# Optimization experiments

Hardware: AMD Instinct MI355X
Metric: run time of the kernel (lower is better)

## Reference

```python
import jax, jax.numpy as jnp
import numpy as np

G, K, H = 4, 8, 512  # gate_dim, k blocks, block size

def setup_inputs() -> dict:
    key = jax.random.key(0)
    kx, kA, kB = jax.random.split(key, 3)
    x = jax.random.normal(kx, (4096, K * H), dtype=jnp.float32)
    # xavier_normal for (h,h) matrices: std = sqrt(2/(h+h)) = 1/sqrt(h)
    std = 1.0 / np.sqrt(H)
    A = jax.random.normal(kA, (G, H, H), dtype=jnp.float32) * std
    B = jax.random.normal(kB, (G, H, H), dtype=jnp.float32) * std
    return {"x": x, "A": A, "B": B}

def reference(x, A, B):
    # W = blockdiag-style: row block (g,i), col block j -> A_g if i==j else B_g.
    # y[b, g, i, :] = x_i @ A_g^T + (sum_j x_j - x_i) @ B_g^T
    #              = x_i @ (A_g - B_g)^T + S @ B_g^T
    bsz = x.shape[0]
    x3 = x.reshape(bsz, K, H)                      # [B, k, h]
    S = x3.sum(axis=1)                              # [B, h]
    diag_part = jnp.einsum('bkh,gph->bgkp', x3, A - B)   # [B, g, k, h]
    sum_part = jnp.einsum('bh,gph->bgp', S, B)           # [B, g, h]
    out = diag_part + sum_part[:, :, None, :]
    return out.reshape(bsz, G * K * H)
```

## Files before the change

### kernel.cpp

```cpp
#include <hip/hip_runtime.h>

typedef _Float16 f16x8 __attribute__((ext_vector_type(8)));
typedef _Float16 f16x4 __attribute__((ext_vector_type(4)));
typedef _Float16 f16x2 __attribute__((ext_vector_type(2)));
typedef float f32x4 __attribute__((ext_vector_type(4)));
typedef float f32x2 __attribute__((ext_vector_type(2)));

#define GLD_LDS16(gp, lp)                                                        \
  __builtin_amdgcn_global_load_lds(                                              \
      (const __attribute__((address_space(1))) void*)(gp),                       \
      (__attribute__((address_space(3))) void*)(lp), 16, 0, 0)

__global__ void prep_weights_k(const float* __restrict__ A, const float* __restrict__ B,
                               _Float16* __restrict__ Cw, _Float16* __restrict__ Bw) {
  int gid = blockIdx.x * 256 + threadIdx.x;
  f32x4 a = ((const f32x4*)A)[gid];
  f32x4 b = ((const f32x4*)B)[gid];
  f16x4 c, bb;
  c.x = (_Float16)(a.x - b.x); c.y = (_Float16)(a.y - b.y);
  c.z = (_Float16)(a.z - b.z); c.w = (_Float16)(a.w - b.w);
  bb.x = (_Float16)b.x; bb.y = (_Float16)b.y;
  bb.z = (_Float16)b.z; bb.w = (_Float16)b.w;
  ((f16x4*)Cw)[gid] = c;
  ((f16x4*)Bw)[gid] = bb;
}

__global__ void prep_x_k(const float* __restrict__ x, _Float16* __restrict__ xh,
                         _Float16* __restrict__ Sh) {
  int b = blockIdx.x, t = threadIdx.x;
  const f32x2* xr = (const f32x2*)(x + (size_t)b * 4096);
  f16x2* xo = (f16x2*)xh + (size_t)b * 2048;
  float s0 = 0.f, s1 = 0.f;
#pragma unroll
  for (int i = 0; i < 8; ++i) {
    f32x2 v = xr[i * 256 + t];
    f16x2 h;
    h.x = (_Float16)v.x; h.y = (_Float16)v.y;
    xo[i * 256 + t] = h;
    s0 += v.x; s1 += v.y;
  }
  f16x2 sv;
  sv.x = (_Float16)s0; sv.y = (_Float16)s1;
  ((f16x2*)Sh)[(size_t)b * 256 + t] = sv;
}

template <int MODE>
__global__ __launch_bounds__(256) void gemm_k(const _Float16* __restrict__ Am,
                                              const _Float16* __restrict__ W,
                                              const float* __restrict__ tvec,
                                              float* __restrict__ out) {
  __shared__ __align__(16) _Float16 lA[128 * 32];
  __shared__ __align__(16) _Float16 lB[128 * 32];

  const int tid = threadIdx.x;
  const int lane = tid & 63;
  const int wv = tid >> 6;
  const int tile_n = blockIdx.x & 15;
  const int tile_m = blockIdx.x >> 4;

  const _Float16* gA[2];
  const _Float16* gB[2];
  _Float16* lpA[2];
  _Float16* lpB[2];
#pragma unroll
  for (int i = 0; i < 2; ++i) {
    int c = i * 256 + tid;
    int row = c >> 2;
    int lc = (c & 3) ^ ((row >> 1) & 3);
    gA[i] = Am + ((size_t)(tile_m * 128 + row) * 512 + lc * 8);
    gB[i] = W + ((size_t)(tile_n * 128 + row) * 512 + lc * 8);
    lpA[i] = &lA[(size_t)(i * 256 + wv * 64) * 8];
    lpB[i] = &lB[(size_t)(i * 256 + wv * 64) * 8];
  }

  const int lm = lane & 15;
  const int q = lane >> 4;
  const int mw = (wv >> 1) * 64;
  const int nw = (wv & 1) * 64;

  int aoff[4], boff[4];
#pragma unroll
  for (int f = 0; f < 4; ++f) {
    int rA = mw + f * 16 + lm;
    aoff[f] = rA * 32 + (q ^ ((rA >> 1) & 3)) * 8;
    int rB = nw + f * 16 + lm;
    boff[f] = rB * 32 + (q ^ ((rB >> 1) & 3)) * 8;
  }

  f32x4 acc[4][4];
#pragma unroll
  for (int im = 0; im < 4; ++im)
#pragma unroll
    for (int in = 0; in < 4; ++in) acc[im][in] = (f32x4){0.f, 0.f, 0.f, 0.f};

  for (int kt = 0; kt < 16; ++kt) {
    __syncthreads();
#pragma unroll
    for (int i = 0; i < 2; ++i) {
      GLD_LDS16(gA[i] + kt * 32, lpA[i]);
      GLD_LDS16(gB[i] + kt * 32, lpB[i]);
    }
    __syncthreads();
    f16x8 af[4], bf[4];
#pragma unroll
    for (int f = 0; f < 4; ++f) {
      af[f] = *(const f16x8*)&lA[aoff[f]];
      bf[f] = *(const f16x8*)&lB[boff[f]];
    }
#pragma unroll
    for (int im = 0; im < 4; ++im)
#pragma unroll
      for (int in = 0; in < 4; ++in)
        acc[im][in] =
            __builtin_amdgcn_mfma_f32_16x16x32_f16(af[im], bf[in], acc[im][in], 0, 0, 0);
  }

#pragma unroll
  for (int im = 0; im < 4; ++im) {
    const int mbase = tile_m * 128 + mw + im * 16 + q * 4;
#pragma unroll
    for (int in = 0; in < 4; ++in) {
      const int col = tile_n * 128 + nw + in * 16 + lm;
      f32x4 v = acc[im][in];
      if (MODE == 1) {
        const int b = mbase >> 3;
        const float tv = tvec[(size_t)b * 2048 + col];
        float* op = out + (size_t)b * 16384 + (size_t)(col >> 9) * 4096 +
                    (size_t)(mbase & 7) * 512 + (col & 511);
#pragma unroll
        for (int r = 0; r < 4; ++r) op[r * 512] = v[r] + tv;
      } else {
        float* op = out + (size_t)mbase * 2048 + col;
#pragma unroll
        for (int r = 0; r < 4; ++r) op[(size_t)r * 2048] = v[r];
      }
    }
  }
}

extern "C" void kernel_launch(void* const* d_in, const int* in_sizes, int n_in,
                              void* d_out, int out_size, void* d_ws, size_t ws_size,
                              hipStream_t stream) {
  const float* x = (const float*)d_in[0];
  const float* A = (const float*)d_in[1];
  const float* B = (const float*)d_in[2];
  float* out = (float*)d_out;
  char* ws = (char*)d_ws;

  _Float16* xh = (_Float16*)(ws);
  _Float16* Sh = (_Float16*)(ws + 33554432u);
  _Float16* Cw = (_Float16*)(ws + 37748736u);
  _Float16* Bw = (_Float16*)(ws + 39845888u);
  float* tv = (float*)(ws + 41943040u);

  prep_weights_k<<<1024, 256, 0, stream>>>(A, B, Cw, Bw);
  prep_x_k<<<4096, 256, 0, stream>>>(x, xh, Sh);
  gemm_k<0><<<512, 256, 0, stream>>>(Sh, Bw, nullptr, tv);
  gemm_k<1><<<4096, 256, 0, stream>>>(xh, Cw, tv, out);
}
```

Before: 420.6 us.

## Fuse the S·B GEMM into the main GEMM epilogue via LDS

Computes the per-batch S@B^T term inside the main GEMM by loading an extra S tile and B weight tile each k-step and issuing two extra MFMAs per wave, then staging the result in LDS and adding it in the epilogue. This removes a separate kernel launch and the global write/read of the intermediate tvec. In exchange each block reloads B tiles and redundantly computes its slice of the sum term, increasing global loads and LDS usage per block.

```diff
diff --git a/kernel.cpp b/kernel.cpp
--- a/kernel.cpp
+++ b/kernel.cpp
@@ -44,13 +44,15 @@
   ((f16x2*)Sh)[(size_t)b * 256 + t] = sv;
 }
 
-template <int MODE>
-__global__ __launch_bounds__(256) void gemm_k(const _Float16* __restrict__ Am,
-                                              const _Float16* __restrict__ W,
-                                              const float* __restrict__ tvec,
-                                              float* __restrict__ out) {
+__global__ __launch_bounds__(256) void gemm_fused_k(const _Float16* __restrict__ Am,
+                                                    const _Float16* __restrict__ Cw,
+                                                    const _Float16* __restrict__ Bw,
+                                                    const _Float16* __restrict__ Sh,
+                                                    float* __restrict__ out) {
   __shared__ __align__(16) _Float16 lA[128 * 32];
-  __shared__ __align__(16) _Float16 lB[128 * 32];
+  __shared__ __align__(16) _Float16 lW[128 * 32];
+  __shared__ __align__(16) _Float16 lV[128 * 32];
+  __shared__ __align__(16) _Float16 lS[16 * 32];
 
   const int tid = threadIdx.x;
   const int lane = tid & 63;
@@ -59,26 +61,32 @@
   const int tile_m = blockIdx.x >> 4;
 
   const _Float16* gA[2];
-  const _Float16* gB[2];
+  const _Float16* gW[2];
+  const _Float16* gV[2];
   _Float16* lpA[2];
-  _Float16* lpB[2];
+  _Float16* lpW[2];
+  _Float16* lpV[2];
 #pragma unroll
   for (int i = 0; i < 2; ++i) {
     int c = i * 256 + tid;
     int row = c >> 2;
     int lc = (c & 3) ^ ((row >> 1) & 3);
     gA[i] = Am + ((size_t)(tile_m * 128 + row) * 512 + lc * 8);
-    gB[i] = W + ((size_t)(tile_n * 128 + row) * 512 + lc * 8);
-    lpA[i] = &lA[(size_t)(i * 256 + wv * 64) * 8];
-    lpB[i] = &lB[(size_t)(i * 256 + wv * 64) * 8];
+    gW[i] = Cw + ((size_t)(tile_n * 128 + row) * 512 + lc * 8);
+    gV[i] = Bw + ((size_t)(tile_n * 128 + row) * 512 + lc * 8);
+    lpA[i] = &lA[(i * 256 + wv * 64) * 8];
+    lpW[i] = &lW[(i * 256 + wv * 64) * 8];
+    lpV[i] = &lV[(i * 256 + wv * 64) * 8];
   }
+  const _Float16* gS =
+      Sh + ((size_t)(tile_m * 16 + (lane >> 2)) * 512 + (lane & 3) * 8);
 
   const int lm = lane & 15;
   const int q = lane >> 4;
   const int mw = (wv >> 1) * 64;
   const int nw = (wv & 1) * 64;
 
-  int aoff[4], boff[4];
+  int aoff[4], boff[4], voff[2];
 #pragma unroll
   for (int f = 0; f < 4; ++f) {
     int rA = mw + f * 16 + lm;
@@ -86,54 +94,78 @@
     int rB = nw + f * 16 + lm;
     boff[f] = rB * 32 + (q ^ ((rB >> 1) & 3)) * 8;
   }
+#pragma unroll
+  for (int f = 0; f < 2; ++f) {
+    int rV = wv * 32 + f * 16 + lm;
+    voff[f] = rV * 32 + (q ^ ((rV >> 1) & 3)) * 8;
+  }
+  const int soff = lm * 32 + q * 8;
 
   f32x4 acc[4][4];
+  f32x4 tacc[2];
 #pragma unroll
   for (int im = 0; im < 4; ++im)
 #pragma unroll
     for (int in = 0; in < 4; ++in) acc[im][in] = (f32x4){0.f, 0.f, 0.f, 0.f};
+#pragma unroll
+  for (int f = 0; f < 2; ++f) tacc[f] = (f32x4){0.f, 0.f, 0.f, 0.f};
 
   for (int kt = 0; kt < 16; ++kt) {
     __syncthreads();
 #pragma unroll
     for (int i = 0; i < 2; ++i) {
       GLD_LDS16(gA[i] + kt * 32, lpA[i]);
-      GLD_LDS16(gB[i] + kt * 32, lpB[i]);
+      GLD_LDS16(gW[i] + kt * 32, lpW[i]);
+      GLD_LDS16(gV[i] + kt * 32, lpV[i]);
     }
+    if (wv == 0) GLD_LDS16(gS + kt * 32, &lS[0]);
     __syncthreads();
-    f16x8 af[4], bf[4];
+    f16x8 af[4], bf[4], vf[2], sf;
+    sf = *(const f16x8*)&lS[soff];
 #pragma unroll
     for (int f = 0; f < 4; ++f) {
       af[f] = *(const f16x8*)&lA[aoff[f]];
-      bf[f] = *(const f16x8*)&lB[boff[f]];
+      bf[f] = *(const f16x8*)&lW[boff[f]];
     }
+#pragma unroll
+    for (int f = 0; f < 2; ++f) vf[f] = *(const f16x8*)&lV[voff[f]];
 #pragma unroll
     for (int im = 0; im < 4; ++im)
 #pragma unroll
       for (int in = 0; in < 4; ++in)
         acc[im][in] =
             __builtin_amdgcn_mfma_f32_16x16x32_f16(af[im], bf[in], acc[im][in], 0, 0, 0);
+#pragma unroll
+    for (int f = 0; f < 2; ++f)
+      tacc[f] = __builtin_amdgcn_mfma_f32_16x16x32_f16(sf, vf[f], tacc[f], 0, 0, 0);
   }
+
+  __syncthreads();
+  float* lT = (float*)lA;
+#pragma unroll
+  for (int f = 0; f < 2; ++f) {
+    int colb = wv * 32 + f * 16 + lm;
+#pragma unroll
+    for (int r = 0; r < 4; ++r) lT[(q * 4 + r) * 128 + colb] = tacc[f][r];
+  }
+  __syncthreads();
 
 #pragma unroll
   for (int im = 0; im < 4; ++im) {
-    const int mbase = tile_m * 128 + mw + im * 16 + q * 4;
+    const int mloc = mw + im * 16 + q * 4;
+    const int mbase = tile_m * 128 + mloc;
+    const int b = mbase >> 3;
+    const int bl = mloc >> 3;
 #pragma unroll
     for (int in = 0; in < 4; ++in) {
-      const int col = tile_n * 128 + nw + in * 16 + lm;
+      const int cl = nw + in * 16 + lm;
+      const int col = tile_n * 128 + cl;
+      const float tv = lT[bl * 128 + cl];
       f32x4 v = acc[im][in];
-      if (MODE == 1) {
-        const int b = mbase >> 3;
-        const float tv = tvec[(size_t)b * 2048 + col];
-        float* op = out + (size_t)b * 16384 + (size_t)(col >> 9) * 4096 +
-                    (size_t)(mbase & 7) * 512 + (col & 511);
+      float* op = out + (size_t)b * 16384 + (size_t)(col >> 9) * 4096 +
+                  (size_t)(mbase & 7) * 512 + (col & 511);
 #pragma unroll
-        for (int r = 0; r < 4; ++r) op[r * 512] = v[r] + tv;
-      } else {
-        float* op = out + (size_t)mbase * 2048 + col;
-#pragma unroll
-        for (int r = 0; r < 4; ++r) op[(size_t)r * 2048] = v[r];
-      }
+      for (int r = 0; r < 4; ++r) op[r * 512] = v[r] + tv;
     }
   }
 }
@@ -151,10 +183,8 @@
   _Float16* Sh = (_Float16*)(ws + 33554432u);
   _Float16* Cw = (_Float16*)(ws + 37748736u);
   _Float16* Bw = (_Float16*)(ws + 39845888u);
-  float* tv = (float*)(ws + 41943040u);
 
   prep_weights_k<<<1024, 256, 0, stream>>>(A, B, Cw, Bw);
   prep_x_k<<<4096, 256, 0, stream>>>(x, xh, Sh);
-  gemm_k<0><<<512, 256, 0, stream>>>(Sh, Bw, nullptr, tv);
-  gemm_k<1><<<4096, 256, 0, stream>>>(xh, Cw, tv, out);
+  gemm_fused_k<<<4096, 256, 0, stream>>>(xh, Cw, Bw, Sh, out);
 }
```

Result: no change. 420.9 us (+0.1%).
